# Kernel optimization log

Measured on AMD Instinct MI355X. Metric: run time of the kernel, lower is better.

The kernel has to match this reference:

```python
import jax, jax.numpy as jnp
import numpy as np

EMBED = 256
HEADS = 8
LEVELS = 1
POINTS = 4
NBQ = 2          # num_bev_queue
HBEV = 128
WBEV = 128
BS = 1


def setup_inputs() -> dict:
    key = jax.random.key(0)
    ks = jax.random.split(key, 10)
    Nq = HBEV * WBEV
    E = EMBED
    so_out = NBQ * HEADS * LEVELS * POINTS * 2
    aw_out = NBQ * HEADS * LEVELS * POINTS
    return {
        "query": jax.random.normal(ks[0], (BS, Nq, E), jnp.float32),
        "value": jax.random.normal(ks[1], (BS, NBQ * Nq, E), jnp.float32),
        "reference_points": jax.random.uniform(ks[2], (BS, Nq, LEVELS, 2), jnp.float32),
        # params stored as [in, out]; y = x @ W + b (math-equivalent to torch Linear)
        "W_vproj": jax.random.normal(ks[3], (E, E), jnp.float32) / np.sqrt(E).astype(np.float32),
        "b_vproj": jnp.zeros((E,), jnp.float32),
        "W_so": jax.random.normal(ks[4], (NBQ * E, so_out), jnp.float32) * 0.01,
        "b_so": jax.random.normal(ks[5], (so_out,), jnp.float32) * 0.5,
        "W_aw": jax.random.normal(ks[6], (NBQ * E, aw_out), jnp.float32) * 0.01,
        "b_aw": jnp.zeros((aw_out,), jnp.float32),
        "W_out": jax.random.normal(ks[7], (E, E), jnp.float32) / np.sqrt(E).astype(np.float32),
        "b_out": jnp.zeros((E,), jnp.float32),
        "spatial_shapes": jnp.array([[HBEV, WBEV]], jnp.int32),
        "level_start_index": jnp.array([0], jnp.int32),
    }


def _msda(value, spatial_shapes, sampling_locations, attention_weights):
    """Multi-scale deformable attention (grid_sample semantics: bilinear,
    zero padding, align_corners=False).
    value: [B, sum(H*W), Hh, d]; sampling_locations: [B, Nq, Hh, L, P, 2] in [0,1];
    attention_weights: [B, Nq, Hh, L, P]. Returns [B, Nq, Hh*d]."""
    B, _, Hh, d = value.shape
    _, Nq, _, L, P, _ = sampling_locations.shape
    ss = np.asarray(spatial_shapes)
    out = jnp.zeros((B, Nq, Hh, d), value.dtype)
    start = 0
    for l in range(L):
        H_, W_ = int(ss[l, 0]), int(ss[l, 1])
        v = value[:, start:start + H_ * W_]          # [B, H*W, Hh, d]
        start += H_ * W_
        loc = sampling_locations[:, :, :, l]          # [B, Nq, Hh, P, 2]
        # align_corners=False: pixel = loc*size - 0.5
        px = loc[..., 0] * W_ - 0.5
        py = loc[..., 1] * H_ - 0.5
        x0f = jnp.floor(px)
        y0f = jnp.floor(py)
        lx = px - x0f
        ly = py - y0f
        x0 = x0f.astype(jnp.int32)
        y0 = y0f.astype(jnp.int32)

        def gather(ix, iy):
            valid = ((ix >= 0) & (ix < W_) & (iy >= 0) & (iy < H_))
            idx = jnp.clip(iy, 0, H_ - 1) * W_ + jnp.clip(ix, 0, W_ - 1)   # [B,Nq,Hh,P]
            idx = jnp.transpose(idx, (0, 1, 3, 2)).reshape(B, Nq * P, Hh, 1)
            g = jnp.take_along_axis(v, idx, axis=1).reshape(B, Nq, P, Hh, d)
            m = jnp.transpose(valid, (0, 1, 3, 2))[..., None].astype(value.dtype)
            return g * m

        def wmul(w):  # [B,Nq,Hh,P] -> [B,Nq,P,Hh,1]
            return jnp.transpose(w, (0, 1, 3, 2))[..., None]

        sampled = (wmul((1 - lx) * (1 - ly)) * gather(x0, y0)
                   + wmul(lx * (1 - ly)) * gather(x0 + 1, y0)
                   + wmul((1 - lx) * ly) * gather(x0, y0 + 1)
                   + wmul(lx * ly) * gather(x0 + 1, y0 + 1))   # [B,Nq,P,Hh,d]
        out = out + jnp.einsum('bqphd,bqhp->bqhd', sampled, attention_weights[:, :, :, l])
    return out.reshape(B, Nq, Hh * d)


def reference(query, value, reference_points, W_vproj, b_vproj, W_so, b_so,
              W_aw, b_aw, W_out, b_out, spatial_shapes, level_start_index):
    bs, Nq, E = query.shape
    Hh, L, P, nbq = HEADS, LEVELS, POINTS, NBQ
    identity = query
    # query enhanced with the previous-BEV slice of value
    qe = jnp.concatenate([value[:, :Nq], query], axis=-1)        # [bs, Nq, 2E]
    v = (value @ W_vproj + b_vproj).reshape(bs * nbq, Nq, Hh, E // Hh)
    so = (qe @ W_so + b_so).reshape(bs, Nq, Hh, nbq, L, P, 2)
    aw = jax.nn.softmax((qe @ W_aw + b_aw).reshape(bs, Nq, Hh, nbq, L * P), axis=-1)
    aw = aw.reshape(bs, Nq, Hh, nbq, L, P)
    aw = jnp.transpose(aw, (0, 3, 1, 2, 4, 5)).reshape(bs * nbq, Nq, Hh, L, P)
    so = jnp.transpose(so, (0, 3, 1, 2, 4, 5, 6)).reshape(bs * nbq, Nq, Hh, L, P, 2)
    rp = jnp.tile(reference_points, (nbq, 1, 1, 1))              # [bs*nbq, Nq, L, 2]
    ssf = spatial_shapes.astype(so.dtype)
    offset_normalizer = jnp.stack([ssf[:, 1], ssf[:, 0]], -1)    # [L, 2] = (W, H)
    loc = rp[:, :, None, :, None, :] + so / offset_normalizer[None, None, None, :, None, :]
    out = _msda(v, spatial_shapes, loc, aw).reshape(bs, nbq, Nq, E).mean(axis=1)
    out = out @ W_out + b_out
    return out + identity  # dropout is identity in eval mode
```

## Files before the change

### kernel.cpp

```cpp
#include <hip/hip_runtime.h>
#include <math.h>

#define NQ     16384
#define GW     128
#define GH     128

typedef __attribute__((ext_vector_type(8))) short short8;
typedef __attribute__((ext_vector_type(4))) float f32x4;

static __device__ __forceinline__ unsigned short f2bf(float f) {
    unsigned u = __builtin_bit_cast(unsigned, f);
    u += 0x7FFFu + ((u >> 16) & 1u);
    return (unsigned short)(u >> 16);
}
static __device__ __forceinline__ unsigned pk2(float lo, float hi) {
    return (unsigned)f2bf(lo) | ((unsigned)f2bf(hi) << 16);
}
static __device__ __forceinline__ float bflo(unsigned u) {
    return __builtin_bit_cast(float, u << 16);
}
static __device__ __forceinline__ float bfhi(unsigned u) {
    return __builtin_bit_cast(float, u & 0xffff0000u);
}

static __device__ __forceinline__ void gload16(const void* g, void* l) {
    __builtin_amdgcn_global_load_lds(
        (const __attribute__((address_space(1))) void*)g,
        (__attribute__((address_space(3))) void*)l, 16, 0, 0);
}

__global__ void prep(const float* __restrict__ Wv, const float* __restrict__ Wso,
                     const float* __restrict__ Waw, const float* __restrict__ bso,
                     const float* __restrict__ baw, const float* __restrict__ Wo,
                     unsigned short* __restrict__ WTv, unsigned short* __restrict__ WTso,
                     unsigned short* __restrict__ WTo, float* __restrict__ bias2)
{
    const int n = blockIdx.x;
    const int k = threadIdx.x;
    WTv[n * 256 + k] = f2bf(Wv[(size_t)k * 256 + n]);
    WTo[n * 256 + k] = f2bf(Wo[(size_t)k * 256 + n]);
    float s0, s1;
    if (n < 128)      { s0 = Wso[(size_t)k * 128 + n];       s1 = Wso[(size_t)(k + 256) * 128 + n]; }
    else if (n < 192) { s0 = Waw[(size_t)k * 64 + n - 128];  s1 = Waw[(size_t)(k + 256) * 64 + n - 128]; }
    else              { s0 = 0.f; s1 = 0.f; }
    WTso[(size_t)n * 512 + k]       = f2bf(s0);
    WTso[(size_t)n * 512 + k + 256] = f2bf(s1);
    if (k == 0) bias2[n] = (n < 128) ? bso[n] : ((n < 192) ? baw[n - 128] : 0.f);
}

template<int KTOT, int MODE>
static __device__ __forceinline__ void gemm_body(
    int m0, int n0,
    const float* __restrict__ A1, const float* __restrict__ A2,
    const unsigned short* __restrict__ Abf,
    const unsigned short* __restrict__ WT,
    const float* __restrict__ bias, const float* __restrict__ resid,
    void* __restrict__ Cout,
    unsigned short* As, unsigned short* Bs)
{
    const int tid = threadIdx.x;
    const int w = tid >> 6, lane = tid & 63;
    const int wr = w >> 1, wc = w & 1;
    const int g = lane >> 4, r16 = lane & 15;
    const int arow = tid >> 3, aoc = tid & 7;
    const int NT = KTOT / 64;

    float4 ra[4];
    f32x4 acc[2][4] = {};

#define SWZ(row, chunk) (((chunk) ^ ((row) & 7)) * 8)

#define STAGE_G(t, bufi)                                                        \
    {                                                                           \
        int k0 = (t) * 64;                                                      \
        unsigned short* Bb = Bs + (bufi) * 128 * 64;                            \
        _Pragma("unroll")                                                       \
        for (int j = 0; j < 4; ++j) {                                           \
            int s = ((w * 4 + j) << 6) + lane;                                  \
            int r = s >> 3;                                                     \
            int c = (s & 7) ^ (r & 7);                                          \
            gload16(&WT[(size_t)(n0 + r) * KTOT + k0 + c * 8],                  \
                    Bb + (((w * 4 + j) << 6) * 8));                             \
        }                                                                       \
        if (MODE == 2) {                                                        \
            unsigned short* Ab = As + (bufi) * 64 * 64;                         \
            _Pragma("unroll")                                                   \
            for (int j = 0; j < 2; ++j) {                                       \
                int s = ((w * 2 + j) << 6) + lane;                              \
                int r = s >> 3;                                                 \
                int c = (s & 7) ^ (r & 7);                                      \
                gload16(&Abf[(size_t)(m0 + r) * 256 + k0 + c * 8],              \
                        Ab + (((w * 2 + j) << 6) * 8));                         \
            }                                                                   \
        }                                                                       \
    }

#define LOAD_A(t)                                                               \
    if (MODE != 2) {                                                            \
        int k0 = (t) * 64;                                                      \
        const float* Asrc = (KTOT == 512 && k0 >= 256) ? (A2 + (k0 - 256))      \
                                                       : (A1 + k0);             \
        _Pragma("unroll")                                                       \
        for (int i = 0; i < 2; ++i) {                                           \
            const float* p = Asrc + (size_t)(m0 + arow + i * 32) * 256          \
                             + aoc * 8;                                         \
            ra[i * 2 + 0] = *(const float4*)p;                                  \
            ra[i * 2 + 1] = *(const float4*)(p + 4);                            \
        }                                                                       \
    }

#define WRITE_A(bufi)                                                           \
    if (MODE != 2) {                                                            \
        unsigned short* Ab = As + (bufi) * 64 * 64;                             \
        _Pragma("unroll")                                                       \
        for (int i = 0; i < 2; ++i) {                                           \
            uint4 wv;                                                           \
            wv.x = pk2(ra[i * 2].x, ra[i * 2].y);                               \
            wv.y = pk2(ra[i * 2].z, ra[i * 2].w);                               \
            wv.z = pk2(ra[i * 2 + 1].x, ra[i * 2 + 1].y);                       \
            wv.w = pk2(ra[i * 2 + 1].z, ra[i * 2 + 1].w);                       \
            int r = arow + i * 32;                                              \
            *(uint4*)&Ab[r * 64 + SWZ(r, aoc)] = wv;                            \
        }                                                                       \
    }

    STAGE_G(0, 0);
    LOAD_A(0);
    WRITE_A(0);
    __syncthreads();

    for (int t = 0; t < NT; ++t) {
        if (t + 1 < NT) { STAGE_G(t + 1, (t + 1) & 1); LOAD_A(t + 1); }
        const unsigned short* Ab = As + (t & 1) * 64 * 64;
        const unsigned short* Bb = Bs + (t & 1) * 128 * 64;
        #pragma unroll
        for (int kh = 0; kh < 2; ++kh) {
            short8 af[2], bfr[4];
            #pragma unroll
            for (int mi = 0; mi < 2; ++mi) {
                int r = wr * 32 + mi * 16 + r16;
                af[mi] = *(const short8*)&Ab[r * 64 + SWZ(r, kh * 4 + g)];
            }
            #pragma unroll
            for (int nj = 0; nj < 4; ++nj) {
                int r = wc * 64 + nj * 16 + r16;
                bfr[nj] = *(const short8*)&Bb[r * 64 + SWZ(r, kh * 4 + g)];
            }
            #pragma unroll
            for (int mi = 0; mi < 2; ++mi)
                #pragma unroll
                for (int nj = 0; nj < 4; ++nj)
                    acc[mi][nj] = __builtin_amdgcn_mfma_f32_16x16x32_bf16(
                        af[mi], bfr[nj], acc[mi][nj], 0, 0, 0);
        }
        if (t + 1 < NT) WRITE_A((t + 1) & 1);
        __syncthreads();
    }
#undef STAGE_G
#undef LOAD_A
#undef WRITE_A
#undef SWZ

    #pragma unroll
    for (int mi = 0; mi < 2; ++mi) {
        int row = m0 + wr * 32 + mi * 16 + g * 4;
        #pragma unroll
        for (int nj = 0; nj < 4; ++nj) {
            int col = n0 + wc * 64 + nj * 16 + r16;
            if (MODE == 1 && col >= 192) continue;
            float bia = bias[col];
            #pragma unroll
            for (int j = 0; j < 4; ++j) {
                float vo = acc[mi][nj][j] + bia;
                if (MODE == 0) {
                    ((unsigned short*)Cout)[(size_t)(row + j) * 256 + col] = f2bf(vo);
                } else if (MODE == 1) {
                    ((float*)Cout)[(size_t)(row + j) * 192 + col] = vo;
                } else {
                    ((float*)Cout)[(size_t)(row + j) * 256 + col] =
                        vo + resid[(size_t)(row + j) * 256 + col];
                }
            }
        }
    }
}

__global__ __launch_bounds__(256)
void gemm_vs(const float* __restrict__ value, const float* __restrict__ query,
             const unsigned short* __restrict__ WTv, const unsigned short* __restrict__ WTso,
             const float* __restrict__ bv, const float* __restrict__ bias2,
             unsigned short* __restrict__ v_out, float* __restrict__ soaw_out)
{
    __shared__ __align__(16) unsigned short As[2 * 64 * 64];
    __shared__ __align__(16) unsigned short Bs[2 * 128 * 64];
    const int bid = blockIdx.x;
    if (bid < 512) {
        gemm_body<512, 1>((bid >> 1) * 64, (bid & 1) * 128,
                          value, query, nullptr, WTso, bias2, nullptr, soaw_out, As, Bs);
    } else {
        const int b2 = bid - 512;
        gemm_body<256, 0>((b2 >> 1) * 64, (b2 & 1) * 128,
                          value, nullptr, nullptr, WTv, bv, nullptr, v_out, As, Bs);
    }
}

__global__ __launch_bounds__(256)
void gemm_out(const unsigned short* __restrict__ Abf, const unsigned short* __restrict__ WTo,
              const float* __restrict__ bo, const float* __restrict__ resid,
              float* __restrict__ out)
{
    __shared__ __align__(16) unsigned short As[2 * 64 * 64];
    __shared__ __align__(16) unsigned short Bs[2 * 128 * 64];
    gemm_body<256, 2>((blockIdx.x >> 1) * 64, (blockIdx.x & 1) * 128,
                      nullptr, nullptr, Abf, WTo, bo, resid, out, As, Bs);
}

static __device__ __forceinline__ void acc8(float* acc, float w, uint4 r) {
    acc[0] = fmaf(w, bflo(r.x), acc[0]);
    acc[1] = fmaf(w, bfhi(r.x), acc[1]);
    acc[2] = fmaf(w, bflo(r.y), acc[2]);
    acc[3] = fmaf(w, bfhi(r.y), acc[3]);
    acc[4] = fmaf(w, bflo(r.z), acc[4]);
    acc[5] = fmaf(w, bfhi(r.z), acc[5]);
    acc[6] = fmaf(w, bflo(r.w), acc[6]);
    acc[7] = fmaf(w, bfhi(r.w), acc[7]);
}

__global__ __launch_bounds__(256)
void sampler(const unsigned short* __restrict__ v, const float* __restrict__ soaw,
             const float* __restrict__ rp, unsigned short* __restrict__ outm)
{
    __shared__ float so_s[4][128];
    __shared__ float w_s[4][64];
    __shared__ float rp_s[4][2];

    const int t = threadIdx.x;
    const int bid = blockIdx.x;
    const int q0 = ((bid & 7) * 512 + (bid >> 3)) * 4;

    #pragma unroll
    for (int i = 0; i < 2; ++i) {
        int idx = t + i * 256;
        int qq = idx >> 7, off = idx & 127;
        so_s[qq][off] = soaw[(size_t)(q0 + qq) * 192 + off];
    }
    if (t < 64) {
        int qq = t >> 4, grp = t & 15;
        float4 a4 = *reinterpret_cast<const float4*>(
            &soaw[(size_t)(q0 + qq) * 192 + 128 + grp * 4]);
        float m = fmaxf(fmaxf(a4.x, a4.y), fmaxf(a4.z, a4.w));
        float e0 = __expf(a4.x - m), e1 = __expf(a4.y - m);
        float e2 = __expf(a4.z - m), e3 = __expf(a4.w - m);
        float inv = 1.f / (e0 + e1 + e2 + e3);
        w_s[qq][grp * 4 + 0] = e0 * inv;
        w_s[qq][grp * 4 + 1] = e1 * inv;
        w_s[qq][grp * 4 + 2] = e2 * inv;
        w_s[qq][grp * 4 + 3] = e3 * inv;
    }
    if (t < 8) rp_s[t >> 1][t & 1] = rp[(size_t)(q0 + (t >> 1)) * 2 + (t & 1)];
    __syncthreads();

    const int wq = t >> 6;
    const int q = q0 + wq;
    const int ln = t & 63;
    const int b = ln >> 5;
    const int s = ln & 31;
    const int h = s >> 2, c = s & 3;
    const int sub = h * 64 + c * 16;
    const float rpx = rp_s[wq][0], rpy = rp_s[wq][1];
    const char* vb = (const char*)v + (size_t)b * NQ * 512;
    float acc[8] = {};

    #pragma unroll
    for (int p = 0; p < 4; ++p) {
        float sox = so_s[wq][h * 16 + b * 8 + p * 2 + 0];
        float soy = so_s[wq][h * 16 + b * 8 + p * 2 + 1];
        float wbp = w_s[wq][h * 8 + b * 4 + p];
        float px = (rpx + sox * (1.0f / 128.0f)) * 128.0f - 0.5f;
        float py = (rpy + soy * (1.0f / 128.0f)) * 128.0f - 0.5f;
        float x0f = floorf(px), y0f = floorf(py);
        float lx = px - x0f, ly = py - y0f;
        int x0 = (int)x0f, y0 = (int)y0f;
        int x1 = x0 + 1, y1 = y0 + 1;
        float wx0 = (1.f - lx) * ((x0 >= 0 && x0 < GW) ? 1.f : 0.f);
        float wx1 = lx         * ((x1 >= 0 && x1 < GW) ? 1.f : 0.f);
        float wy0 = (1.f - ly) * ((y0 >= 0 && y0 < GH) ? 1.f : 0.f);
        float wy1 = ly         * ((y1 >= 0 && y1 < GH) ? 1.f : 0.f);
        int x0c = min(max(x0, 0), GW - 1), x1c = min(max(x1, 0), GW - 1);
        int y0c = min(max(y0, 0), GH - 1), y1c = min(max(y1, 0), GH - 1);
        uint4 r00 = *(const uint4*)(vb + ((size_t)(y0c * GW + x0c) * 512 + sub));
        uint4 r10 = *(const uint4*)(vb + ((size_t)(y0c * GW + x1c) * 512 + sub));
        uint4 r01 = *(const uint4*)(vb + ((size_t)(y1c * GW + x0c) * 512 + sub));
        uint4 r11 = *(const uint4*)(vb + ((size_t)(y1c * GW + x1c) * 512 + sub));
        acc8(acc, wbp * wx0 * wy0, r00);
        acc8(acc, wbp * wx1 * wy0, r10);
        acc8(acc, wbp * wx0 * wy1, r01);
        acc8(acc, wbp * wx1 * wy1, r11);
    }

    #pragma unroll
    for (int i = 0; i < 8; ++i) acc[i] += __shfl_xor(acc[i], 32);

    if (b == 0) {
        uint4 o;
        o.x = pk2(0.5f * acc[0], 0.5f * acc[1]);
        o.y = pk2(0.5f * acc[2], 0.5f * acc[3]);
        o.z = pk2(0.5f * acc[4], 0.5f * acc[5]);
        o.w = pk2(0.5f * acc[6], 0.5f * acc[7]);
        *reinterpret_cast<uint4*>((char*)outm + (size_t)q * 512 + sub) = o;
    }
}

extern "C" void kernel_launch(void* const* d_in, const int* in_sizes, int n_in,
                              void* d_out, int out_size, void* d_ws, size_t ws_size,
                              hipStream_t stream)
{
    const float* query   = (const float*)d_in[0];
    const float* value   = (const float*)d_in[1];
    const float* rp      = (const float*)d_in[2];
    const float* W_vproj = (const float*)d_in[3];
    const float* b_vproj = (const float*)d_in[4];
    const float* W_so    = (const float*)d_in[5];
    const float* b_so    = (const float*)d_in[6];
    const float* W_aw    = (const float*)d_in[7];
    const float* b_aw    = (const float*)d_in[8];
    const float* W_out   = (const float*)d_in[9];
    const float* b_out   = (const float*)d_in[10];
    float* out = (float*)d_out;

    char* wp = (char*)d_ws;
    unsigned short* ws_v    = (unsigned short*)wp; wp += (size_t)2 * NQ * 256 * 2;
    float*          ws_soaw = (float*)wp;          wp += (size_t)NQ * 192 * 4;
    unsigned short* ws_mean = (unsigned short*)wp; wp += (size_t)NQ * 256 * 2;
    unsigned short* WTv     = (unsigned short*)wp; wp += 256 * 256 * 2;
    unsigned short* WTso    = (unsigned short*)wp; wp += 256 * 512 * 2;
    unsigned short* WTo     = (unsigned short*)wp; wp += 256 * 256 * 2;
    float*          bias2   = (float*)wp;          wp += 256 * 4;

    prep<<<dim3(256), dim3(256), 0, stream>>>(W_vproj, W_so, W_aw, b_so, b_aw, W_out,
                                              WTv, WTso, WTo, bias2);
    gemm_vs<<<dim3(1536), dim3(256), 0, stream>>>(value, query, WTv, WTso,
                                                  b_vproj, bias2, ws_v, ws_soaw);
    sampler<<<dim3(NQ / 4), dim3(256), 0, stream>>>(ws_v, ws_soaw, rp, ws_mean);
    gemm_out<<<dim3(512), dim3(256), 0, stream>>>(ws_mean, WTo, b_out, query, out);
}
```

Baseline: 79.46 us.

## Fuse deformable sampler with output projection GEMM and drop LDS-direct loads

Merges the sampler and the output-projection GEMM into one kernel. Each 512-thread block samples 16 queries, keeps their bf16 mean in LDS and runs MFMA against WTo read straight from global memory, then adds bias and residual. This removes the intermediate mean buffer round trip and one launch. Separately, the shared GEMM body swaps global_load_lds staging of the B tile for register loads followed by swizzled LDS writes. Risks: WTo is re-read from global by every block with no LDS staging, fewer blocks run in the fused stage, and the register-staged B path may lose the async copy overlap.

```diff
diff --git a/kernel.cpp b/kernel.cpp
--- a/kernel.cpp
+++ b/kernel.cpp
@@ -21,12 +21,6 @@
 }
 static __device__ __forceinline__ float bfhi(unsigned u) {
     return __builtin_bit_cast(float, u & 0xffff0000u);
-}
-
-static __device__ __forceinline__ void gload16(const void* g, void* l) {
-    __builtin_amdgcn_global_load_lds(
-        (const __attribute__((address_space(1))) void*)g,
-        (__attribute__((address_space(3))) void*)l, 16, 0, 0);
 }
 
 __global__ void prep(const float* __restrict__ Wv, const float* __restrict__ Wso,
@@ -52,9 +46,8 @@
 static __device__ __forceinline__ void gemm_body(
     int m0, int n0,
     const float* __restrict__ A1, const float* __restrict__ A2,
-    const unsigned short* __restrict__ Abf,
     const unsigned short* __restrict__ WT,
-    const float* __restrict__ bias, const float* __restrict__ resid,
+    const float* __restrict__ bias,
     void* __restrict__ Cout,
     unsigned short* As, unsigned short* Bs)
 {
@@ -66,37 +59,11 @@
     const int NT = KTOT / 64;
 
     float4 ra[4];
+    uint4  rb[4];
     f32x4 acc[2][4] = {};
 
-#define SWZ(row, chunk) (((chunk) ^ ((row) & 7)) * 8)
-
-#define STAGE_G(t, bufi)                                                        \
+#define LOAD_T(t)                                                               \
     {                                                                           \
-        int k0 = (t) * 64;                                                      \
-        unsigned short* Bb = Bs + (bufi) * 128 * 64;                            \
-        _Pragma("unroll")                                                       \
-        for (int j = 0; j < 4; ++j) {                                           \
-            int s = ((w * 4 + j) << 6) + lane;                                  \
-            int r = s >> 3;                                                     \
-            int c = (s & 7) ^ (r & 7);                                          \
-            gload16(&WT[(size_t)(n0 + r) * KTOT + k0 + c * 8],                  \
-                    Bb + (((w * 4 + j) << 6) * 8));                             \
-        }                                                                       \
-        if (MODE == 2) {                                                        \
-            unsigned short* Ab = As + (bufi) * 64 * 64;                         \
-            _Pragma("unroll")                                                   \
-            for (int j = 0; j < 2; ++j) {                                       \
-                int s = ((w * 2 + j) << 6) + lane;                              \
-                int r = s >> 3;                                                 \
-                int c = (s & 7) ^ (r & 7);                                      \
-                gload16(&Abf[(size_t)(m0 + r) * 256 + k0 + c * 8],              \
-                        Ab + (((w * 2 + j) << 6) * 8));                         \
-            }                                                                   \
-        }                                                                       \
-    }
-
-#define LOAD_A(t)                                                               \
-    if (MODE != 2) {                                                            \
         int k0 = (t) * 64;                                                      \
         const float* Asrc = (KTOT == 512 && k0 >= 256) ? (A2 + (k0 - 256))      \
                                                        : (A1 + k0);             \
@@ -107,11 +74,18 @@
             ra[i * 2 + 0] = *(const float4*)p;                                  \
             ra[i * 2 + 1] = *(const float4*)(p + 4);                            \
         }                                                                       \
-    }
-
-#define WRITE_A(bufi)                                                           \
-    if (MODE != 2) {                                                            \
+        _Pragma("unroll")                                                       \
+        for (int i = 0; i < 4; ++i)                                             \
+            rb[i] = *(const uint4*)&WT[(size_t)(n0 + arow + i * 32) * KTOT      \
+                                       + k0 + aoc * 8];                         \
+    }
+
+#define SWZ(row, chunk) (((chunk) ^ ((row) & 7)) * 8)
+
+#define WRITE_T(bufi)                                                           \
+    {                                                                           \
         unsigned short* Ab = As + (bufi) * 64 * 64;                             \
+        unsigned short* Bb = Bs + (bufi) * 128 * 64;                            \
         _Pragma("unroll")                                                       \
         for (int i = 0; i < 2; ++i) {                                           \
             uint4 wv;                                                           \
@@ -122,15 +96,19 @@
             int r = arow + i * 32;                                              \
             *(uint4*)&Ab[r * 64 + SWZ(r, aoc)] = wv;                            \
         }                                                                       \
-    }
-
-    STAGE_G(0, 0);
-    LOAD_A(0);
-    WRITE_A(0);
+        _Pragma("unroll")                                                       \
+        for (int i = 0; i < 4; ++i) {                                           \
+            int r = arow + i * 32;                                              \
+            *(uint4*)&Bb[r * 64 + SWZ(r, aoc)] = rb[i];                         \
+        }                                                                       \
+    }
+
+    LOAD_T(0);
+    WRITE_T(0);
     __syncthreads();
 
     for (int t = 0; t < NT; ++t) {
-        if (t + 1 < NT) { STAGE_G(t + 1, (t + 1) & 1); LOAD_A(t + 1); }
+        if (t + 1 < NT) LOAD_T(t + 1);
         const unsigned short* Ab = As + (t & 1) * 64 * 64;
         const unsigned short* Bb = Bs + (t & 1) * 128 * 64;
         #pragma unroll
@@ -153,12 +131,11 @@
                     acc[mi][nj] = __builtin_amdgcn_mfma_f32_16x16x32_bf16(
                         af[mi], bfr[nj], acc[mi][nj], 0, 0, 0);
         }
-        if (t + 1 < NT) WRITE_A((t + 1) & 1);
+        if (t + 1 < NT) WRITE_T((t + 1) & 1);
         __syncthreads();
     }
-#undef STAGE_G
-#undef LOAD_A
-#undef WRITE_A
+#undef LOAD_T
+#undef WRITE_T
 #undef SWZ
 
     #pragma unroll
@@ -174,11 +151,8 @@
                 float vo = acc[mi][nj][j] + bia;
                 if (MODE == 0) {
                     ((unsigned short*)Cout)[(size_t)(row + j) * 256 + col] = f2bf(vo);
-                } else if (MODE == 1) {
+                } else {
                     ((float*)Cout)[(size_t)(row + j) * 192 + col] = vo;
-                } else {
-                    ((float*)Cout)[(size_t)(row + j) * 256 + col] =
-                        vo + resid[(size_t)(row + j) * 256 + col];
                 }
             }
         }
@@ -196,23 +170,12 @@
     const int bid = blockIdx.x;
     if (bid < 512) {
         gemm_body<512, 1>((bid >> 1) * 64, (bid & 1) * 128,
-                          value, query, nullptr, WTso, bias2, nullptr, soaw_out, As, Bs);
+                          value, query, WTso, bias2, soaw_out, As, Bs);
     } else {
         const int b2 = bid - 512;
         gemm_body<256, 0>((b2 >> 1) * 64, (b2 & 1) * 128,
-                          value, nullptr, nullptr, WTv, bv, nullptr, v_out, As, Bs);
-    }
-}
-
-__global__ __launch_bounds__(256)
-void gemm_out(const unsigned short* __restrict__ Abf, const unsigned short* __restrict__ WTo,
-              const float* __restrict__ bo, const float* __restrict__ resid,
-              float* __restrict__ out)
-{
-    __shared__ __align__(16) unsigned short As[2 * 64 * 64];
-    __shared__ __align__(16) unsigned short Bs[2 * 128 * 64];
-    gemm_body<256, 2>((blockIdx.x >> 1) * 64, (blockIdx.x & 1) * 128,
-                      nullptr, nullptr, Abf, WTo, bo, resid, out, As, Bs);
+                          value, nullptr, WTv, bv, v_out, As, Bs);
+    }
 }
 
 static __device__ __forceinline__ void acc8(float* acc, float w, uint4 r) {
@@ -226,88 +189,127 @@
     acc[7] = fmaf(w, bfhi(r.w), acc[7]);
 }
 
-__global__ __launch_bounds__(256)
-void sampler(const unsigned short* __restrict__ v, const float* __restrict__ soaw,
-             const float* __restrict__ rp, unsigned short* __restrict__ outm)
-{
-    __shared__ float so_s[4][128];
-    __shared__ float w_s[4][64];
-    __shared__ float rp_s[4][2];
+__global__ __launch_bounds__(512)
+void fused_so(const unsigned short* __restrict__ v, const float* __restrict__ soaw,
+              const float* __restrict__ rp, const unsigned short* __restrict__ WTo,
+              const float* __restrict__ bo, const float* __restrict__ query,
+              float* __restrict__ out)
+{
+    __shared__ float so_s[8][128];
+    __shared__ float w_s[8][64];
+    __shared__ float rp_s[8][2];
+    __shared__ __align__(16) unsigned short mean_lds[16 * 256];
 
     const int t = threadIdx.x;
     const int bid = blockIdx.x;
-    const int q0 = ((bid & 7) * 512 + (bid >> 3)) * 4;
-
-    #pragma unroll
-    for (int i = 0; i < 2; ++i) {
-        int idx = t + i * 256;
-        int qq = idx >> 7, off = idx & 127;
-        so_s[qq][off] = soaw[(size_t)(q0 + qq) * 192 + off];
-    }
-    if (t < 64) {
-        int qq = t >> 4, grp = t & 15;
-        float4 a4 = *reinterpret_cast<const float4*>(
-            &soaw[(size_t)(q0 + qq) * 192 + 128 + grp * 4]);
-        float m = fmaxf(fmaxf(a4.x, a4.y), fmaxf(a4.z, a4.w));
-        float e0 = __expf(a4.x - m), e1 = __expf(a4.y - m);
-        float e2 = __expf(a4.z - m), e3 = __expf(a4.w - m);
-        float inv = 1.f / (e0 + e1 + e2 + e3);
-        w_s[qq][grp * 4 + 0] = e0 * inv;
-        w_s[qq][grp * 4 + 1] = e1 * inv;
-        w_s[qq][grp * 4 + 2] = e2 * inv;
-        w_s[qq][grp * 4 + 3] = e3 * inv;
-    }
-    if (t < 8) rp_s[t >> 1][t & 1] = rp[(size_t)(q0 + (t >> 1)) * 2 + (t & 1)];
-    __syncthreads();
-
+    const int q0 = ((bid & 7) * 128 + (bid >> 3)) * 16;
     const int wq = t >> 6;
-    const int q = q0 + wq;
     const int ln = t & 63;
-    const int b = ln >> 5;
+    const int bb = ln >> 5;
     const int s = ln & 31;
     const int h = s >> 2, c = s & 3;
     const int sub = h * 64 + c * 16;
-    const float rpx = rp_s[wq][0], rpy = rp_s[wq][1];
-    const char* vb = (const char*)v + (size_t)b * NQ * 512;
-    float acc[8] = {};
-
+
+    for (int ps = 0; ps < 2; ++ps) {
+        const int qb = ps * 8;
+        #pragma unroll
+        for (int i = 0; i < 2; ++i) {
+            int idx = t + i * 512;
+            int qq = idx >> 7, off = idx & 127;
+            so_s[qq][off] = soaw[(size_t)(q0 + qb + qq) * 192 + off];
+        }
+        if (t < 128) {
+            int qq = t >> 4, grp = t & 15;
+            float4 a4 = *reinterpret_cast<const float4*>(
+                &soaw[(size_t)(q0 + qb + qq) * 192 + 128 + grp * 4]);
+            float m = fmaxf(fmaxf(a4.x, a4.y), fmaxf(a4.z, a4.w));
+            float e0 = __expf(a4.x - m), e1 = __expf(a4.y - m);
+            float e2 = __expf(a4.z - m), e3 = __expf(a4.w - m);
+            float inv = 1.f / (e0 + e1 + e2 + e3);
+            w_s[qq][grp * 4 + 0] = e0 * inv;
+            w_s[qq][grp * 4 + 1] = e1 * inv;
+            w_s[qq][grp * 4 + 2] = e2 * inv;
+            w_s[qq][grp * 4 + 3] = e3 * inv;
+        }
+        if (t < 16) rp_s[t >> 1][t & 1] = rp[(size_t)(q0 + qb + (t >> 1)) * 2 + (t & 1)];
+        __syncthreads();
+
+        const int qlocal = qb + wq;
+        const float rpx = rp_s[wq][0], rpy = rp_s[wq][1];
+        const char* vb = (const char*)v + (size_t)bb * NQ * 512;
+        float acc[8] = {};
+
+        #pragma unroll
+        for (int p = 0; p < 4; ++p) {
+            float sox = so_s[wq][h * 16 + bb * 8 + p * 2 + 0];
+            float soy = so_s[wq][h * 16 + bb * 8 + p * 2 + 1];
+            float wbp = w_s[wq][h * 8 + bb * 4 + p];
+            float px = (rpx + sox * (1.0f / 128.0f)) * 128.0f - 0.5f;
+            float py = (rpy + soy * (1.0f / 128.0f)) * 128.0f - 0.5f;
+            float x0f = floorf(px), y0f = floorf(py);
+            float lx = px - x0f, ly = py - y0f;
+            int x0 = (int)x0f, y0 = (int)y0f;
+            int x1 = x0 + 1, y1 = y0 + 1;
+            float wx0 = (1.f - lx) * ((x0 >= 0 && x0 < GW) ? 1.f : 0.f);
+            float wx1 = lx         * ((x1 >= 0 && x1 < GW) ? 1.f : 0.f);
+            float wy0 = (1.f - ly) * ((y0 >= 0 && y0 < GH) ? 1.f : 0.f);
+            float wy1 = ly         * ((y1 >= 0 && y1 < GH) ? 1.f : 0.f);
+            int x0c = min(max(x0, 0), GW - 1), x1c = min(max(x1, 0), GW - 1);
+            int y0c = min(max(y0, 0), GH - 1), y1c = min(max(y1, 0), GH - 1);
+            uint4 r00 = *(const uint4*)(vb + ((size_t)(y0c * GW + x0c) * 512 + sub));
+            uint4 r10 = *(const uint4*)(vb + ((size_t)(y0c * GW + x1c) * 512 + sub));
+            uint4 r01 = *(const uint4*)(vb + ((size_t)(y1c * GW + x0c) * 512 + sub));
+            uint4 r11 = *(const uint4*)(vb + ((size_t)(y1c * GW + x1c) * 512 + sub));
+            acc8(acc, wbp * wx0 * wy0, r00);
+            acc8(acc, wbp * wx1 * wy0, r10);
+            acc8(acc, wbp * wx0 * wy1, r01);
+            acc8(acc, wbp * wx1 * wy1, r11);
+        }
+
+        #pragma unroll
+        for (int i = 0; i < 8; ++i) acc[i] += __shfl_xor(acc[i], 32);
+
+        if (bb == 0) {
+            uint4 o;
+            o.x = pk2(0.5f * acc[0], 0.5f * acc[1]);
+            o.y = pk2(0.5f * acc[2], 0.5f * acc[3]);
+            o.z = pk2(0.5f * acc[4], 0.5f * acc[5]);
+            o.w = pk2(0.5f * acc[6], 0.5f * acc[7]);
+            int chunk = h * 4 + c;
+            *reinterpret_cast<uint4*>(
+                &mean_lds[qlocal * 256 + ((chunk ^ (qlocal & 7)) * 8)]) = o;
+        }
+        __syncthreads();
+    }
+
+    const int g = ln >> 4, r16 = ln & 15;
+    f32x4 acc2[2] = {};
     #pragma unroll
-    for (int p = 0; p < 4; ++p) {
-        float sox = so_s[wq][h * 16 + b * 8 + p * 2 + 0];
-        float soy = so_s[wq][h * 16 + b * 8 + p * 2 + 1];
-        float wbp = w_s[wq][h * 8 + b * 4 + p];
-        float px = (rpx + sox * (1.0f / 128.0f)) * 128.0f - 0.5f;
-        float py = (rpy + soy * (1.0f / 128.0f)) * 128.0f - 0.5f;
-        float x0f = floorf(px), y0f = floorf(py);
-        float lx = px - x0f, ly = py - y0f;
-        int x0 = (int)x0f, y0 = (int)y0f;
-        int x1 = x0 + 1, y1 = y0 + 1;
-        float wx0 = (1.f - lx) * ((x0 >= 0 && x0 < GW) ? 1.f : 0.f);
-        float wx1 = lx         * ((x1 >= 0 && x1 < GW) ? 1.f : 0.f);
-        float wy0 = (1.f - ly) * ((y0 >= 0 && y0 < GH) ? 1.f : 0.f);
-        float wy1 = ly         * ((y1 >= 0 && y1 < GH) ? 1.f : 0.f);
-        int x0c = min(max(x0, 0), GW - 1), x1c = min(max(x1, 0), GW - 1);
-        int y0c = min(max(y0, 0), GH - 1), y1c = min(max(y1, 0), GH - 1);
-        uint4 r00 = *(const uint4*)(vb + ((size_t)(y0c * GW + x0c) * 512 + sub));
-        uint4 r10 = *(const uint4*)(vb + ((size_t)(y0c * GW + x1c) * 512 + sub));
-        uint4 r01 = *(const uint4*)(vb + ((size_t)(y1c * GW + x0c) * 512 + sub));
-        uint4 r11 = *(const uint4*)(vb + ((size_t)(y1c * GW + x1c) * 512 + sub));
-        acc8(acc, wbp * wx0 * wy0, r00);
-        acc8(acc, wbp * wx1 * wy0, r10);
-        acc8(acc, wbp * wx0 * wy1, r01);
-        acc8(acc, wbp * wx1 * wy1, r11);
-    }
-
+    for (int kh = 0; kh < 8; ++kh) {
+        short8 af;
+        {
+            int chunk = kh * 4 + g;
+            af = *reinterpret_cast<const short8*>(
+                &mean_lds[r16 * 256 + ((chunk ^ (r16 & 7)) * 8)]);
+        }
+        #pragma unroll
+        for (int nj = 0; nj < 2; ++nj) {
+            int col = wq * 32 + nj * 16 + r16;
+            short8 bfv = *reinterpret_cast<const short8*>(
+                &WTo[(size_t)col * 256 + kh * 32 + g * 8]);
+            acc2[nj] = __builtin_amdgcn_mfma_f32_16x16x32_bf16(af, bfv, acc2[nj], 0, 0, 0);
+        }
+    }
     #pragma unroll
-    for (int i = 0; i < 8; ++i) acc[i] += __shfl_xor(acc[i], 32);
-
-    if (b == 0) {
-        uint4 o;
-        o.x = pk2(0.5f * acc[0], 0.5f * acc[1]);
-        o.y = pk2(0.5f * acc[2], 0.5f * acc[3]);
-        o.z = pk2(0.5f * acc[4], 0.5f * acc[5]);
-        o.w = pk2(0.5f * acc[6], 0.5f * acc[7]);
-        *reinterpret_cast<uint4*>((char*)outm + (size_t)q * 512 + sub) = o;
+    for (int nj = 0; nj < 2; ++nj) {
+        int col = wq * 32 + nj * 16 + r16;
+        float bia = bo[col];
+        #pragma unroll
+        for (int j = 0; j < 4; ++j) {
+            int row = q0 + g * 4 + j;
+            out[(size_t)row * 256 + col] =
+                acc2[nj][j] + bia + query[(size_t)row * 256 + col];
+        }
     }
 }
 
@@ -331,7 +333,6 @@
     char* wp = (char*)d_ws;
     unsigned short* ws_v    = (unsigned short*)wp; wp += (size_t)2 * NQ * 256 * 2;
     float*          ws_soaw = (float*)wp;          wp += (size_t)NQ * 192 * 4;
-    unsigned short* ws_mean = (unsigned short*)wp; wp += (size_t)NQ * 256 * 2;
     unsigned short* WTv     = (unsigned short*)wp; wp += 256 * 256 * 2;
     unsigned short* WTso    = (unsigned short*)wp; wp += 256 * 512 * 2;
     unsigned short* WTo     = (unsigned short*)wp; wp += 256 * 256 * 2;
@@ -341,6 +342,6 @@
                                               WTv, WTso, WTo, bias2);
     gemm_vs<<<dim3(1536), dim3(256), 0, stream>>>(value, query, WTv, WTso,
                                                   b_vproj, bias2, ws_v, ws_soaw);
-    sampler<<<dim3(NQ / 4), dim3(256), 0, stream>>>(ws_v, ws_soaw, rp, ws_mean);
-    gemm_out<<<dim3(512), dim3(256), 0, stream>>>(ws_mean, WTo, b_out, query, out);
-}
+    fused_so<<<dim3(1024), dim3(512), 0, stream>>>(ws_v, ws_soaw, rp, WTo,
+                                                   b_out, query, out);
+}
```

New measurement: 79.65 us. Within noise of the previous version (+0.2%).
